# Kernel optimization log

Measured on AMD Instinct MI355X. Metric: run time of the kernel, lower is better.

The kernel has to match this reference:

```python
import math
import jax, jax.numpy as jnp
import numpy as np

N_ORDERS = 2
CHUNK = 64  # tokens per chunk (before virtual-token expansion)


def _expand_derivative(x, n):
    """expand_virtual_tokens(mode='derivative'): [B,H,S,D] -> [B,H,S*n,D]."""
    B, H, S, D = x.shape
    pad = jnp.zeros((B, H, n - 1, D), x.dtype)
    xp = jnp.concatenate([pad, x], axis=2)  # [B,H,S+n-1,D]
    coeffs = np.array([(-1) ** kk * math.comb(n - 1, kk) for kk in range(n)], dtype=np.float32)
    coeffs = coeffs / np.abs(coeffs).sum()  # L1-normalized binomial coeffs
    # window j at token t is x_pad[t+j]*coeffs[j]; then flip window dim (as in torch .flip(-1))
    win = jnp.stack([xp[:, :, j:j + S, :] * coeffs[j] for j in range(n)], axis=3)  # [B,H,S,n,D]
    win = win[:, :, :, ::-1, :]
    return win.reshape(B, H, S * n, D)


def _unlinear(x, scale=2.0):
    """unlinear_activation: gated norm-scaled gelu applied to inter-chunk state."""
    xn = jnp.linalg.norm(x, axis=-1, keepdims=True) + 1e-6
    return x / scale * jax.nn.gelu(scale * x / xn, approximate=True)


def _stab(x):
    # ensure_stability: clamp to [-1e4, 1e4], nan -> center (0)
    return jnp.nan_to_num(jnp.clip(x, -1e4, 1e4), nan=0.0, posinf=1e4, neginf=-1e4)


def _forward(q, k, v, beta):
    n = N_ORDERS
    B, H, S, D = q.shape
    qe = _expand_derivative(q, n)
    ke = _expand_derivative(k, n)
    ve = _expand_derivative(v, n)
    be = jnp.repeat(beta, n, axis=-1)[..., None]  # [B,H,S*n,1]
    w = ke * be  # delta-rule write keys
    u = ve * be  # delta-rule write values

    Cn = CHUNK * n                     # virtual tokens per chunk
    NC = (S * n) // Cn                 # number of chunks
    ch = lambda x: x.reshape(B, H, NC, Cn, D)
    qc, kc, wc, uc = ch(qe), ch(ke), ch(w), ch(u)

    # triangular (forward-substitution) inversion per chunk:
    # T = (I + tril(W K^T, -1))^{-1}  == fast_invert_matrix of the strictly-lower system
    A = jnp.tril(jnp.einsum('bhnid,bhnjd->bhnij', wc, kc), -1)
    eye = jnp.eye(Cn, dtype=q.dtype)
    T = jax.scipy.linalg.solve_triangular(
        eye + A, jnp.broadcast_to(eye, A.shape), lower=True, unit_diagonal=True)
    wci = jnp.einsum('bhnij,bhnjd->bhnid', T, wc)
    uci = jnp.einsum('bhnij,bhnjd->bhnid', T, uc)

    def chunk_step(h, xs):
        # sequential_delta_product_scan body: per-token Householder updates, n_orders steps
        qx, wx, ux = xs  # each [B,H,Cn,D]
        C = CHUNK
        qr = qx.reshape(B, H, C, n, D)
        wr = wx.reshape(B, H, C, n, D)
        ur = ux.reshape(B, H, C, n, D)
        state = jnp.broadcast_to(h[:, :, None], (B, H, C, D, D))  # per-token state
        outs = []
        for s in range(n):
            qs, ws, us = qr[:, :, :, s], wr[:, :, :, s], ur[:, :, :, s]
            kho = jnp.einsum('bhcd,bhcde->bhce', ws, state)
            uval = us - kho
            o_inter = jnp.einsum('bhcd,bhcde->bhce', qs, state)
            o_intra = qs * uval
            state = _stab(state + jnp.einsum('bhcd,bhce->bhcde', ws, uval))
            outs.append(o_intra + o_inter)
        o = jnp.stack(outs, axis=3).reshape(B, H, C * n, D)  # interleave: pos t*n+s
        h_new = _unlinear(state[:, :, -1])  # linear_activation=False path
        return h_new, o

    xs = (jnp.moveaxis(qc, 2, 0), jnp.moveaxis(wci, 2, 0), jnp.moveaxis(uci, 2, 0))
    h0 = jnp.zeros((B, H, D, D), q.dtype)
    _, os = jax.lax.scan(chunk_step, h0, xs)  # os: [NC,B,H,Cn,D]
    out_v = jnp.moveaxis(os, 0, 2).reshape(B, H, S, n, D)
    return out_v[..., n - 1, :]  # collapse virtual tokens: keep last-order output per token


def setup_inputs() -> dict:
    key = jax.random.key(0)
    kq, kk, kv, kb = jax.random.split(key, 4)
    B, H, S, D = 2, 16, 2048, 64
    return {
        'q': jax.random.normal(kq, (B, H, S, D), jnp.float32),
        'k': jax.random.normal(kk, (B, H, S, D), jnp.float32),
        'v': jax.random.normal(kv, (B, H, S, D), jnp.float32),
        'beta': jax.random.uniform(kb, (B, H, S), jnp.float32),
    }


def reference(q, k, v, beta):
    return _forward(q, k, v, beta)
```

## Files before the change

kernel.cpp:

```cpp
#include <hip/hip_runtime.h>
#include <math.h>


namespace {
constexpr int PAIRS = 32;
constexpr int SLEN  = 2048;
constexpr int D     = 64;
constexpr int CK    = 64;
constexpr int CN    = 128;
constexpr int NCH   = 32;
constexpr int NB2   = 16;
constexpr int NP    = 5;

__device__ __forceinline__ float stab1(float x) {
    float y = __builtin_amdgcn_fmed3f(x, -10000.f, 10000.f);
    return (x != x) ? 0.f : y;
}

__device__ __forceinline__ int kidx(int a, int f4) {
    return a * 68 + 4 * (f4 ^ ((a >> 2) & 3));
}
}

__global__ __launch_bounds__(512, 1)
void la_phase1(const float* __restrict__ kg, const float* __restrict__ vg,
               const float* __restrict__ bg, float* __restrict__ ws)
{
    __shared__ float Ysh[CN][CN];
    __shared__ float Gm[65][66];
    __shared__ char  ureg[36864];
    __shared__ float bq4[CK], bh[CK];

    float* kstf = (float*)ureg;
    float* scm  = (float*)ureg;
    float (*redsh)[3][8][CN] = (float(*)[3][8][CN])(ureg + 12288);

    const int blk  = blockIdx.x;
    const int p    = blk >> 5;
    const int nc   = blk & 31;
    const int tid  = threadIdx.x;
    const int baseT = nc * CK;
    const float* kp = kg + (size_t)p * SLEN * D;
    const float* vp = vg + (size_t)p * SLEN * D;
    const float* bp = bg + (size_t)p * SLEN;

    for (int u = tid; u < 65 * 16; u += 512) {
        int a = u >> 4, f4 = u & 15;
        int src = baseT - 1 + a;
        float4 val = float4{0.f, 0.f, 0.f, 0.f};
        if (src >= 0) val = ((const float4*)(kp + (size_t)src * D))[f4];
        *(float4*)&kstf[kidx(a, f4)] = val;
    }
    if (tid < CK) {
        float bv = bp[baseT + tid];
        bq4[tid] = 0.25f * bv;
        bh[tid]  = 0.5f  * bv;
    }
    __syncthreads();

    for (int u = tid; u < CN * 32; u += 512) {
        int i = u >> 5, f4i = u & 31;
        int ci = i >> 1, si = i & 1;
        float sc = si ? bh[ci] : -bh[ci];
        float4 val = float4{0.f, 0.f, 0.f, 0.f};
        if (f4i < 16) {
            val = *(const float4*)&kstf[kidx(ci - si + 1, f4i)];
        } else {
            int srcT = baseT + ci - si;
            if (srcT >= 0) val = ((const float4*)(vp + (size_t)srcT * D))[f4i - 16];
        }
        val.x *= sc; val.y *= sc; val.z *= sc; val.w *= sc;
        *(float4*)&Ysh[i][f4i * 4] = val;
    }

    for (int tt = tid; tt < 17 * 17; tt += 512) {
        int ta = tt / 17, tb = tt % 17;
        if (tb > ta) continue;
        int a0 = ta * 4, b0 = tb * 4;
        float acc[4][4] = {};
        for (int d4 = 0; d4 < 16; ++d4) {
            float4 av[4], bv[4];
            #pragma unroll
            for (int r = 0; r < 4; ++r) {
                av[r] = *(const float4*)&kstf[kidx(min(a0 + r, 64), d4)];
                bv[r] = *(const float4*)&kstf[kidx(min(b0 + r, 64), d4)];
            }
            #pragma unroll
            for (int r = 0; r < 4; ++r)
                #pragma unroll
                for (int c = 0; c < 4; ++c)
                    acc[r][c] += av[r].x * bv[c].x + av[r].y * bv[c].y
                               + av[r].z * bv[c].z + av[r].w * bv[c].w;
        }
        #pragma unroll
        for (int r = 0; r < 4; ++r)
            #pragma unroll
            for (int c = 0; c < 4; ++c)
                if (a0 + r <= 64 && b0 + c <= 64) {
                    Gm[a0 + r][b0 + c] = acc[r][c];
                    Gm[b0 + c][a0 + r] = acc[r][c];
                }
    }
    __syncthreads();

    for (int e = tid; e < 192; e += 512) {
        int gp = (e < 64) ? 0 : 1;
        int ee = e - gp * 64;
        int j = ee >> 3, r = ee & 7;
        int i = 8 * gp + r;
        int ai = (i >> 1) - (i & 1) + 1;
        int aj = (j >> 1) - (j & 1) + 1;
        float sgn = ((i ^ j) & 1) ? -1.f : 1.f;
        scm[(gp * CN + j) * 8 + r] = sgn * bq4[i >> 1] * Gm[ai][aj];
    }
    __syncthreads();

    const int col = tid & 127;
    const int grp = tid >> 7;

    for (int g = 0; g < 16; ++g) {
        const int bufG  = g % 3;
        const int bufG1 = (g + 1) % 3;
        const int bufG2 = (g + 2) % 3;

        if (grp == 0) {
            float acc[8] = {};
            if (g > 0) {
                #pragma unroll
                for (int r = 0; r < 8; ++r)
                    acc[r] = redsh[g & 1][0][r][col] + redsh[g & 1][1][r][col]
                           + redsh[g & 1][2][r][col];
                #pragma unroll
                for (int jj = 0; jj < 8; ++jj) {
                    int j = 8 * g - 8 + jj;
                    float yv = Ysh[j][col];
                    const float4 a03 = *(const float4*)&scm[(bufG * CN + j) * 8];
                    const float4 a47 = *(const float4*)&scm[(bufG * CN + j) * 8 + 4];
                    acc[0] += a03.x * yv; acc[1] += a03.y * yv;
                    acc[2] += a03.z * yv; acc[3] += a03.w * yv;
                    acc[4] += a47.x * yv; acc[5] += a47.y * yv;
                    acc[6] += a47.z * yv; acc[7] += a47.w * yv;
                }
            }
            float yn[8];
            #pragma unroll
            for (int r = 0; r < 8; ++r) {
                float val = Ysh[8 * g + r][col] - acc[r];
                #pragma unroll
                for (int rp = 0; rp < 8; ++rp)
                    if (rp < r) val -= scm[(bufG * CN + 8 * g + rp) * 8 + r] * yn[rp];
                yn[r] = val;
                Ysh[8 * g + r][col] = val;
            }
        } else {
            if (g + 2 <= 15) {
                int gb = g + 2, jmax = 8 * gb + 8;
                for (int e = tid - 128; e < 8 * jmax; e += 384) {
                    int j = e >> 3, r = e & 7;
                    int i = 8 * gb + r;
                    int ai = (i >> 1) - (i & 1) + 1;
                    int aj = (j >> 1) - (j & 1) + 1;
                    float sgn = ((i ^ j) & 1) ? -1.f : 1.f;
                    scm[(bufG2 * CN + j) * 8 + r] = sgn * bq4[i >> 1] * Gm[ai][aj];
                }
            }
            if (g + 1 <= 15) {
                float acc[8] = {};
                for (int j = grp - 1; j < 8 * g; j += 3) {
                    float yv = Ysh[j][col];
                    const float4 a03 = *(const float4*)&scm[(bufG1 * CN + j) * 8];
                    const float4 a47 = *(const float4*)&scm[(bufG1 * CN + j) * 8 + 4];
                    acc[0] += a03.x * yv; acc[1] += a03.y * yv;
                    acc[2] += a03.z * yv; acc[3] += a03.w * yv;
                    acc[4] += a47.x * yv; acc[5] += a47.y * yv;
                    acc[6] += a47.z * yv; acc[7] += a47.w * yv;
                }
                #pragma unroll
                for (int r = 0; r < 8; ++r)
                    redsh[(g + 1) & 1][grp - 1][r][col] = acc[r];
            }
        }
        __syncthreads();
    }

    float* gY = ws + (size_t)(p * NCH + nc) * (CN * CN);
    for (int u = tid; u < CN * 32; u += 512) {
        int r = u >> 5, f4 = u & 31;
        *(float4*)&gY[r * CN + f4 * 4] = *(const float4*)&Ysh[r][f4 * 4];
    }
}

__global__ __launch_bounds__(512, 2)
void la_phase2(const float* __restrict__ qg, const float* __restrict__ ws,
               float* __restrict__ outg)
{
    __shared__ float WU[2][NP][256];
    __shared__ float Qs[2][NP][64];
    __shared__ float partA[8][NP][64];
    __shared__ float partB[8][NP][64];
    __shared__ float UV0[NP][64];
    __shared__ float UV1r[64];

    const int blk  = blockIdx.x;
    const int p    = blk >> 4, nb = blk & 15;
    const int tid  = threadIdx.x;
    const int w    = tid >> 6, lane = tid & 63;

    const float* qp = qg + (size_t)p * SLEN * D;
    float* op = outg + (size_t)p * SLEN * D;
    const float* wsbase = ws + (size_t)p * NCH * (CN * CN);

    const int cMain = nb * 4 + w;

    float4 wuR = float4{0.f, 0.f, 0.f, 0.f};
    float  qR  = 0.f;

    auto stage_load = [&](int nc) {
        const float* gY = wsbase + (size_t)nc * (CN * CN);
        if (w < 4) {
            wuR = *(const float4*)(gY + (size_t)(2 * cMain) * CN + lane * 4);
            int t = nc * CK + cMain;
            qR = qp[(size_t)((t > 0) ? t - 1 : 0) * D + lane];
        } else if (w == 4) {
            wuR = *(const float4*)(gY + (size_t)126 * CN + lane * 4);
            qR = qp[(size_t)(nc * CK + 62) * D + lane];
        }
    };
    auto stage_write = [&](int buf) {
        if (w < NP) {
            *(float4*)&WU[buf][w][lane * 4] = wuR;
            Qs[buf][w][lane] = qR;
        }
    };

    float hs[8];
    #pragma unroll
    for (int j = 0; j < 8; ++j) hs[j] = 0.f;

    stage_load(0);
    stage_write(0);
    __syncthreads();

    for (int nc = 0; nc < NCH; ++nc) {
        const int buf = nc & 1;
        if (nc + 1 < NCH) stage_load(nc + 1);

        #pragma unroll
        for (int P = 0; P < NP; ++P) {
            float4 a = *(const float4*)&WU[buf][P][8 * w];
            float4 b = *(const float4*)&WU[buf][P][8 * w + 4];
            float s = ((a.x * hs[0] + a.y * hs[1]) + (a.z * hs[2] + a.w * hs[3]))
                    + ((b.x * hs[4] + b.y * hs[5]) + (b.z * hs[6] + b.w * hs[7]));
            partA[w][P][lane] = s;
        }
        __syncthreads();

        if (w < NP) {
            float s = 0.f;
            #pragma unroll
            for (int wv = 0; wv < 8; ++wv) s += partA[wv][w][lane];
            UV0[w][lane] = WU[buf][w][64 + lane] - s;
        }
        __syncthreads();

        #pragma unroll
        for (int P = 0; P < NP; ++P) {
            float uv0 = UV0[P][lane];
            float4 w0a = *(const float4*)&WU[buf][P][8 * w];
            float4 w0b = *(const float4*)&WU[buf][P][8 * w + 4];
            float4 w1a = *(const float4*)&WU[buf][P][128 + 8 * w];
            float4 w1b = *(const float4*)&WU[buf][P][128 + 8 * w + 4];
            float4 qa  = *(const float4*)&Qs[buf][P][8 * w];
            float4 qb  = *(const float4*)&Qs[buf][P][8 * w + 4];
            float st0 = stab1(hs[0] + w0a.x * uv0);
            float st1 = stab1(hs[1] + w0a.y * uv0);
            float st2 = stab1(hs[2] + w0a.z * uv0);
            float st3 = stab1(hs[3] + w0a.w * uv0);
            float st4 = stab1(hs[4] + w0b.x * uv0);
            float st5 = stab1(hs[5] + w0b.y * uv0);
            float st6 = stab1(hs[6] + w0b.z * uv0);
            float st7 = stab1(hs[7] + w0b.w * uv0);
            float kh = ((w1a.x * st0 + w1a.y * st1) + (w1a.z * st2 + w1a.w * st3))
                     + ((w1b.x * st4 + w1b.y * st5) + (w1b.z * st6 + w1b.w * st7));
            float oa = ((qa.x * st0 + qa.y * st1) + (qa.z * st2 + qa.w * st3))
                     + ((qb.x * st4 + qb.y * st5) + (qb.z * st6 + qb.w * st7));
            partA[w][P][lane] = kh;
            partB[w][P][lane] = oa;
        }
        __syncthreads();

        if (w < 4) {
            float skh = 0.f, soa = 0.f;
            #pragma unroll
            for (int wv = 0; wv < 8; ++wv) {
                skh += partA[wv][w][lane];
                soa += partB[wv][w][lane];
            }
            float uv1 = WU[buf][w][192 + lane] - skh;
            int t = nc * CK + cMain;
            float outv = 0.5f * (Qs[buf][w][lane] * uv1 + soa);
            op[(size_t)t * D + lane] = (t > 0) ? outv : 0.f;
        } else if (w == 4) {
            float skh = 0.f;
            #pragma unroll
            for (int wv = 0; wv < 8; ++wv) skh += partA[wv][4][lane];
            UV1r[lane] = WU[buf][4][192 + lane] - skh;
        }
        __syncthreads();

        {
            float uv0l = UV0[4][lane];
            float uv1l = UV1r[lane];
            float4 w0a = *(const float4*)&WU[buf][4][8 * w];
            float4 w0b = *(const float4*)&WU[buf][4][8 * w + 4];
            float4 w1a = *(const float4*)&WU[buf][4][128 + 8 * w];
            float4 w1b = *(const float4*)&WU[buf][4][128 + 8 * w + 4];
            float st2v[8], ss[8];
            st2v[0] = stab1(stab1(hs[0] + w0a.x * uv0l) + w1a.x * uv1l);
            st2v[1] = stab1(stab1(hs[1] + w0a.y * uv0l) + w1a.y * uv1l);
            st2v[2] = stab1(stab1(hs[2] + w0a.z * uv0l) + w1a.z * uv1l);
            st2v[3] = stab1(stab1(hs[3] + w0a.w * uv0l) + w1a.w * uv1l);
            st2v[4] = stab1(stab1(hs[4] + w0b.x * uv0l) + w1b.x * uv1l);
            st2v[5] = stab1(stab1(hs[5] + w0b.y * uv0l) + w1b.y * uv1l);
            st2v[6] = stab1(stab1(hs[6] + w0b.z * uv0l) + w1b.z * uv1l);
            st2v[7] = stab1(stab1(hs[7] + w0b.w * uv0l) + w1b.w * uv1l);
            #pragma unroll
            for (int j = 0; j < 8; ++j) ss[j] = st2v[j] * st2v[j];
            #pragma unroll
            for (int msk = 1; msk < 64; msk <<= 1) {
                #pragma unroll
                for (int j = 0; j < 8; ++j) ss[j] += __shfl_xor(ss[j], msk);
            }
            #pragma unroll
            for (int j = 0; j < 8; ++j) {
                float xn = __builtin_amdgcn_sqrtf(ss[j]) + 1e-6f;
                float y  = 2.f * st2v[j] * __builtin_amdgcn_rcpf(xn);
                float y2 = y * y;
                float e  = __builtin_amdgcn_exp2f(y * (2.3022078f + 0.1029432f * y2));
                float th = (e - 1.f) * __builtin_amdgcn_rcpf(e + 1.f);
                hs[j] = 0.25f * st2v[j] * y * (1.f + th);
            }
        }

        if (nc + 1 < NCH) stage_write(buf ^ 1);
        __syncthreads();
    }
}

extern "C" void kernel_launch(void* const* d_in, const int* in_sizes, int n_in,
                              void* d_out, int out_size, void* d_ws, size_t ws_size,
                              hipStream_t stream)
{
    (void)in_sizes; (void)n_in; (void)out_size; (void)ws_size;
    const float* q    = (const float*)d_in[0];
    const float* k    = (const float*)d_in[1];
    const float* v    = (const float*)d_in[2];
    const float* beta = (const float*)d_in[3];
    float* ws  = (float*)d_ws;
    float* out = (float*)d_out;

    la_phase1<<<PAIRS * NCH, 512, 0, stream>>>(k, v, beta, ws);
    la_phase2<<<PAIRS * NB2, 512, 0, stream>>>(q, ws, out);
}
```

Before: 320.6 us.

## Cut per-chunk barriers in phase2 via redundant per-warp reductions

```diff
diff --git a/kernel.cpp b/kernel.cpp
--- a/kernel.cpp
+++ b/kernel.cpp
@@ -190,16 +190,15 @@
     }
 }
 
-__global__ __launch_bounds__(512, 2)
+__global__ __launch_bounds__(512, 4)
 void la_phase2(const float* __restrict__ qg, const float* __restrict__ ws,
                float* __restrict__ outg)
 {
     __shared__ float WU[2][NP][256];
     __shared__ float Qs[2][NP][64];
-    __shared__ float partA[8][NP][64];
-    __shared__ float partB[8][NP][64];
-    __shared__ float UV0[NP][64];
-    __shared__ float UV1r[64];
+    __shared__ float pR1[8][NP][64];
+    __shared__ float pKH[8][NP][64];
+    __shared__ float pOA[8][NP][64];
 
     const int blk  = blockIdx.x;
     const int p    = blk >> 4, nb = blk & 15;
@@ -249,23 +248,24 @@
         for (int P = 0; P < NP; ++P) {
             float4 a = *(const float4*)&WU[buf][P][8 * w];
             float4 b = *(const float4*)&WU[buf][P][8 * w + 4];
-            float s = ((a.x * hs[0] + a.y * hs[1]) + (a.z * hs[2] + a.w * hs[3]))
-                    + ((b.x * hs[4] + b.y * hs[5]) + (b.z * hs[6] + b.w * hs[7]));
-            partA[w][P][lane] = s;
+            pR1[w][P][lane] =
+                  ((a.x * hs[0] + a.y * hs[1]) + (a.z * hs[2] + a.w * hs[3]))
+                + ((b.x * hs[4] + b.y * hs[5]) + (b.z * hs[6] + b.w * hs[7]));
         }
         __syncthreads();
 
-        if (w < NP) {
+        float uv0r[NP];
+        #pragma unroll
+        for (int P = 0; P < NP; ++P) {
             float s = 0.f;
             #pragma unroll
-            for (int wv = 0; wv < 8; ++wv) s += partA[wv][w][lane];
-            UV0[w][lane] = WU[buf][w][64 + lane] - s;
-        }
-        __syncthreads();
+            for (int wv = 0; wv < 8; ++wv) s += pR1[wv][P][lane];
+            uv0r[P] = WU[buf][P][64 + lane] - s;
+        }
 
         #pragma unroll
         for (int P = 0; P < NP; ++P) {
-            float uv0 = UV0[P][lane];
+            float uv0 = uv0r[P];
             float4 w0a = *(const float4*)&WU[buf][P][8 * w];
             float4 w0b = *(const float4*)&WU[buf][P][8 * w + 4];
             float4 w1a = *(const float4*)&WU[buf][P][128 + 8 * w];
@@ -280,37 +280,36 @@
             float st5 = stab1(hs[5] + w0b.y * uv0);
             float st6 = stab1(hs[6] + w0b.z * uv0);
             float st7 = stab1(hs[7] + w0b.w * uv0);
-            float kh = ((w1a.x * st0 + w1a.y * st1) + (w1a.z * st2 + w1a.w * st3))
-                     + ((w1b.x * st4 + w1b.y * st5) + (w1b.z * st6 + w1b.w * st7));
-            float oa = ((qa.x * st0 + qa.y * st1) + (qa.z * st2 + qa.w * st3))
-                     + ((qb.x * st4 + qb.y * st5) + (qb.z * st6 + qb.w * st7));
-            partA[w][P][lane] = kh;
-            partB[w][P][lane] = oa;
-        }
+            pKH[w][P][lane] =
+                  ((w1a.x * st0 + w1a.y * st1) + (w1a.z * st2 + w1a.w * st3))
+                + ((w1b.x * st4 + w1b.y * st5) + (w1b.z * st6 + w1b.w * st7));
+            pOA[w][P][lane] =
+                  ((qa.x * st0 + qa.y * st1) + (qa.z * st2 + qa.w * st3))
+                + ((qb.x * st4 + qb.y * st5) + (qb.z * st6 + qb.w * st7));
+        }
+        stage_write(buf ^ 1);
         __syncthreads();
 
         if (w < 4) {
             float skh = 0.f, soa = 0.f;
             #pragma unroll
             for (int wv = 0; wv < 8; ++wv) {
-                skh += partA[wv][w][lane];
-                soa += partB[wv][w][lane];
+                skh += pKH[wv][w][lane];
+                soa += pOA[wv][w][lane];
             }
             float uv1 = WU[buf][w][192 + lane] - skh;
             int t = nc * CK + cMain;
             float outv = 0.5f * (Qs[buf][w][lane] * uv1 + soa);
             op[(size_t)t * D + lane] = (t > 0) ? outv : 0.f;
-        } else if (w == 4) {
-            float skh = 0.f;
-            #pragma unroll
-            for (int wv = 0; wv < 8; ++wv) skh += partA[wv][4][lane];
-            UV1r[lane] = WU[buf][4][192 + lane] - skh;
-        }
-        __syncthreads();
+        }
+
+        float skh4 = 0.f;
+        #pragma unroll
+        for (int wv = 0; wv < 8; ++wv) skh4 += pKH[wv][4][lane];
+        const float uv1l = WU[buf][4][192 + lane] - skh4;
+        const float uv0l = uv0r[4];
 
         {
-            float uv0l = UV0[4][lane];
-            float uv1l = UV1r[lane];
             float4 w0a = *(const float4*)&WU[buf][4][8 * w];
             float4 w0b = *(const float4*)&WU[buf][4][8 * w + 4];
             float4 w1a = *(const float4*)&WU[buf][4][128 + 8 * w];
@@ -341,9 +340,6 @@
                 hs[j] = 0.25f * st2v[j] * y * (1.f + th);
             }
         }
-
-        if (nc + 1 < NCH) stage_write(buf ^ 1);
-        __syncthreads();
     }
 }
 
```

Measured after the change: 322.9 us. No clear change (+0.7%).
